# Kernel optimization log

Hardware: AMD Instinct MI355X
Metric: run time of the kernel (lower is better)

Reference implementation:

```python
import jax, jax.numpy as jnp
import numpy as np

DIM = 512
NL = 4
P = 8
B = 4
L = 8192  # byte-level sequence length
LP = L // P  # patch-level sequence length


def _ln(x, g, b, eps=1e-5):
    m = jnp.mean(x, axis=-1, keepdims=True)
    v = jnp.mean((x - m) ** 2, axis=-1, keepdims=True)
    return (x - m) * jax.lax.rsqrt(v + eps) * g + b


def setup_inputs() -> dict:
    key = jax.random.key(0)
    ks = jax.random.split(key, 24)
    s = 0.02
    inp = {
        "bytes_in": jax.random.randint(ks[0], (B, L), 0, 256, dtype=jnp.int32),
        "byte_emb": jax.random.normal(ks[1], (256, DIM), jnp.float32) * s,
        # patch encoder Conv1d(kernel=stride=P): weight laid out [P, D_in, D_out]
        "enc_w": jax.random.normal(ks[2], (P, DIM, DIM), jnp.float32) * s,
        "enc_b": jnp.zeros((DIM,), jnp.float32),
        "hash_proj": jax.random.normal(ks[3], (DIM, DIM), jnp.float32) * s,
        # per-layer stacked params
        "qkv_w": jax.random.normal(ks[4], (NL, DIM, 3 * DIM), jnp.float32) * s,
        "qkv_b": jnp.zeros((NL, 3 * DIM), jnp.float32),
        "gate_w": jax.random.normal(ks[5], (NL, DIM, DIM), jnp.float32) * s,
        "gate_b": jnp.zeros((NL, DIM), jnp.float32),
        "ln1_g": jnp.ones((NL, DIM), jnp.float32),
        "ln1_b": jnp.zeros((NL, DIM), jnp.float32),
        "mlp_w1": jax.random.normal(ks[6], (NL, DIM, 4 * DIM), jnp.float32) * s,
        "mlp_b1": jnp.zeros((NL, 4 * DIM), jnp.float32),
        "mlp_w2": jax.random.normal(ks[7], (NL, 4 * DIM, DIM), jnp.float32) * s,
        "mlp_b2": jnp.zeros((NL, DIM), jnp.float32),
        "ln2_g": jnp.ones((NL, DIM), jnp.float32),
        "ln2_b": jnp.zeros((NL, DIM), jnp.float32),
        # patch decoder ConvTranspose1d(kernel=stride=P): weight [D_in, P, D_out]
        "dec_w": jax.random.normal(ks[8], (DIM, P, DIM), jnp.float32) * s,
        "dec_b": jnp.zeros((DIM,), jnp.float32),
        "head_w": jax.random.normal(ks[9], (DIM, 256), jnp.float32) * s,
        "head_b": jnp.zeros((256,), jnp.float32),
    }
    return inp


def reference(bytes_in, byte_emb, enc_w, enc_b, hash_proj,
              qkv_w, qkv_b, gate_w, gate_b, ln1_g, ln1_b,
              mlp_w1, mlp_b1, mlp_w2, mlp_b2, ln2_g, ln2_b,
              dec_w, dec_b, head_w, head_b):
    # byte embedding: [B, L, D]
    x = byte_emb[bytes_in]
    # non-overlapping Conv1d(kernel=stride=P) == patch-wise contraction
    xp = x.reshape(B, LP, P, DIM)
    x = jnp.einsum('blpd,pdo->blo', xp, enc_w) + enc_b  # [B, LP, D]
    # hash projection
    x = x + jnp.tanh(x @ hash_proj)
    for i in range(NL):
        # LinearLatentKernel
        h = _ln(x, ln1_g[i], ln1_b[i])
        qkv = h @ qkv_w[i] + qkv_b[i]
        q, k, v = jnp.split(qkv, 3, axis=-1)
        kv_state = jnp.cumsum(k * v, axis=1)
        g = jax.nn.sigmoid(h @ gate_w[i] + gate_b[i])
        x = x + q * kv_state * g
        # MLP
        h = _ln(x, ln2_g[i], ln2_b[i])
        h = jax.nn.gelu(h @ mlp_w1[i] + mlp_b1[i], approximate=False)
        x = x + h @ mlp_w2[i] + mlp_b2[i]
    # ConvTranspose1d(kernel=stride=P): each patch expands to P positions
    y = jnp.einsum('bld,dpo->blpo', x, dec_w).reshape(B, L, DIM) + dec_b
    logits = y @ head_w + head_b  # [B, L, 256]
    return logits
```

## Files before the change

### kernel.cpp

```cpp
#include <hip/hip_runtime.h>
#include <hip/hip_bf16.h>
#include <math.h>

#define DIMD 512
#define NLAYER 4
#define PP 8
#define BBATCH 4
#define LBYTES 8192
#define LPATCH 1024
#define MROWS (BBATCH * LPATCH)

typedef __bf16 bf16x8 __attribute__((ext_vector_type(8)));
typedef float f32x4 __attribute__((ext_vector_type(4)));
typedef unsigned short u16x4 __attribute__((ext_vector_type(4)));
typedef unsigned short u16x8 __attribute__((ext_vector_type(8)));

__device__ __forceinline__ unsigned short f2bf(float f) {
    union { float f; unsigned u; } v; v.f = f;
    unsigned r = v.u + 0x7FFFu + ((v.u >> 16) & 1u);
    return (unsigned short)(r >> 16);
}
__device__ __forceinline__ float bf2f(unsigned short u) {
    union { unsigned u; float f; } v; v.u = ((unsigned)u) << 16;
    return v.f;
}

__device__ __forceinline__ void glds16(const unsigned short* g, unsigned short* l) {
    __builtin_amdgcn_global_load_lds((__attribute__((address_space(1))) void*)g,
                                     (__attribute__((address_space(3))) void*)l,
                                     16, 0, 0);
}

template<int TM, int ACT, bool BIAS, bool RES, bool OBF>
__global__ __launch_bounds__(256)
void mfma_gemm(const unsigned short* __restrict__ A, int lda, long aZ,
               const unsigned short* __restrict__ Bt, int ldb, long bZ,
               const float* __restrict__ bias,
               const float* __restrict__ res, int ldr,
               void* __restrict__ Cv, int ldc, long cZ, int K)
{
    constexpr int M_REP = TM / 32;
    __shared__ unsigned short As[TM * 32];
    __shared__ unsigned short Bs[128 * 32];

    const int tid = threadIdx.x;
    const int w = tid >> 6, l = tid & 63;
    const int row0 = blockIdx.x * TM;
    const int col0 = blockIdx.y * 128;
    A  += (size_t)blockIdx.z * aZ;
    Bt += (size_t)blockIdx.z * bZ;
    unsigned short* Cb = (unsigned short*)Cv + (size_t)blockIdx.z * cZ;
    float*          Cf = (float*)Cv          + (size_t)blockIdx.z * cZ;

    const int cA = w * 64 + l;
    const unsigned short* gA0 = A + (size_t)(row0 + (cA >> 2)) * lda + (cA & 3) * 8;
    const unsigned short* gB0 = Bt + (size_t)(col0 + (cA >> 2)) * ldb + (cA & 3) * 8;
    const unsigned short* gB1 = Bt + (size_t)(col0 + 64 + (cA >> 2)) * ldb + (cA & 3) * 8;
    unsigned short* lA0 = &As[w * 512];
    unsigned short* lB0 = &Bs[w * 512];
    unsigned short* lB1 = &Bs[2048 + w * 512];
    const unsigned short* gA1 = nullptr;
    unsigned short* lA1 = nullptr;
    if constexpr (TM == 128) {
        gA1 = A + (size_t)(row0 + 64 + (cA >> 2)) * lda + (cA & 3) * 8;
        lA1 = &As[2048 + w * 512];
    }

    const int wr = (w >> 1) * (TM / 2);
    const int wc = (w & 1) * 64;
    const int lr = l & 15, lk = (l >> 4) * 8;
    const int aBase = (wr + lr) * 32 + lk;
    const int bBase = (wc + lr) * 32 + lk;

    f32x4 acc[M_REP][4] = {};

    for (int k0 = 0; k0 < K; k0 += 32) {
        glds16(gA0, lA0);  gA0 += 32;
        if constexpr (TM == 128) { glds16(gA1, lA1); gA1 += 32; }
        glds16(gB0, lB0);  gB0 += 32;
        glds16(gB1, lB1);  gB1 += 32;
        __syncthreads();
        bf16x8 af[M_REP], bfr[4];
        #pragma unroll
        for (int m = 0; m < M_REP; m++)
            af[m] = *reinterpret_cast<const bf16x8*>(&As[aBase + m * 512]);
        #pragma unroll
        for (int n = 0; n < 4; n++)
            bfr[n] = *reinterpret_cast<const bf16x8*>(&Bs[bBase + n * 512]);
        #pragma unroll
        for (int m = 0; m < M_REP; m++)
            #pragma unroll
            for (int n = 0; n < 4; n++)
                acc[m][n] = __builtin_amdgcn_mfma_f32_16x16x32_bf16(
                    af[m], bfr[n], acc[m][n], 0, 0, 0);
        __syncthreads();
    }

    const int r0 = row0 + wr + (l >> 4) * 4;
    const int c0 = col0 + wc + lr;
    float bv[4] = {0.f, 0.f, 0.f, 0.f};
    if (BIAS) {
        #pragma unroll
        for (int n = 0; n < 4; n++) bv[n] = bias[c0 + n * 16];
    }
    #pragma unroll
    for (int m = 0; m < M_REP; m++) {
        #pragma unroll
        for (int j = 0; j < 4; j++) {
            const int row = r0 + m * 16 + j;
            #pragma unroll
            for (int n = 0; n < 4; n++) {
                float v = acc[m][n][j];
                if (BIAS) v += bv[n];
                if (ACT == 1) v = tanhf(v);
                if (ACT == 2) v = 0.5f * v * (1.f + erff(v * 0.70710678118f));
                if (RES) v += res[(size_t)row * ldr + c0 + n * 16];
                if (OBF) Cb[(size_t)row * ldc + c0 + n * 16] = f2bf(v);
                else     Cf[(size_t)row * ldc + c0 + n * 16] = v;
            }
        }
    }
}

__global__ __launch_bounds__(256)
void pack_t(const float* __restrict__ in, unsigned short* __restrict__ out,
            int K, int N, long inZ, long outZ)
{
    __shared__ float t[32][33];
    const int k0 = blockIdx.x * 32, n0 = blockIdx.y * 32;
    in  += (size_t)blockIdx.z * inZ;
    out += (size_t)blockIdx.z * outZ;
    const int tx = threadIdx.x & 31, ty = threadIdx.x >> 5;
    #pragma unroll
    for (int i = 0; i < 4; i++)
        t[ty + i * 8][tx] = in[(size_t)(k0 + ty + i * 8) * N + n0 + tx];
    __syncthreads();
    #pragma unroll
    for (int i = 0; i < 4; i++)
        out[(size_t)(n0 + ty + i * 8) * K + k0 + tx] = f2bf(t[tx][ty + i * 8]);
}

__global__ __launch_bounds__(256)
void ln_kernel(const float* __restrict__ x, const float* __restrict__ g,
               const float* __restrict__ b, unsigned short* __restrict__ h)
{
    const int row = blockIdx.x * 4 + (threadIdx.x >> 6);
    const int lane = threadIdx.x & 63;
    const float* xr = x + (long)row * DIMD;
    float4 v0 = *(const float4*)(xr + lane * 8);
    float4 v1 = *(const float4*)(xr + lane * 8 + 4);
    float xv[8] = {v0.x, v0.y, v0.z, v0.w, v1.x, v1.y, v1.z, v1.w};
    float s = 0.f, q = 0.f;
    #pragma unroll
    for (int j = 0; j < 8; j++) { s += xv[j]; q += xv[j] * xv[j]; }
    #pragma unroll
    for (int off = 1; off < 64; off <<= 1) {
        s += __shfl_xor(s, off);
        q += __shfl_xor(q, off);
    }
    const float mean = s * (1.f / DIMD);
    const float var  = q * (1.f / DIMD) - mean * mean;
    const float rstd = rsqrtf(var + 1e-5f);
    float4 g0 = *(const float4*)(g + lane * 8);
    float4 g1 = *(const float4*)(g + lane * 8 + 4);
    float4 b0 = *(const float4*)(b + lane * 8);
    float4 b1 = *(const float4*)(b + lane * 8 + 4);
    float gv[8] = {g0.x, g0.y, g0.z, g0.w, g1.x, g1.y, g1.z, g1.w};
    float bb[8] = {b0.x, b0.y, b0.z, b0.w, b1.x, b1.y, b1.z, b1.w};
    u16x8 o;
    #pragma unroll
    for (int j = 0; j < 8; j++) o[j] = f2bf((xv[j] - mean) * rstd * gv[j] + bb[j]);
    *reinterpret_cast<u16x8*>(h + (long)row * DIMD + lane * 8) = o;
}

__global__ __launch_bounds__(128)
void embed_kernel(const int* __restrict__ bytes, const float* __restrict__ E,
                  const float* __restrict__ enc_b, float* __restrict__ x0,
                  unsigned short* __restrict__ x0b)
{
    const int patch = blockIdx.x;
    __shared__ int by[PP];
    if (threadIdx.x < PP) by[threadIdx.x] = bytes[patch * PP + threadIdx.x];
    __syncthreads();
    const int o = threadIdx.x * 4;
    float4 acc = *(const float4*)(enc_b + o);
    #pragma unroll
    for (int p = 0; p < PP; p++) {
        float4 e = *(const float4*)(E + ((long)(p * 256 + by[p])) * DIMD + o);
        acc.x += e.x; acc.y += e.y; acc.z += e.z; acc.w += e.w;
    }
    *(float4*)(x0 + (long)patch * DIMD + o) = acc;
    u16x4 ob; ob[0] = f2bf(acc.x); ob[1] = f2bf(acc.y);
    ob[2] = f2bf(acc.z); ob[3] = f2bf(acc.w);
    *reinterpret_cast<u16x4*>(x0b + (long)patch * DIMD + o) = ob;
}

#define NCHUNK 64
#define CLEN   16
#define QGS    (4 * DIMD)

__global__ __launch_bounds__(512)
void scan_partial(const unsigned short* __restrict__ qg, float* __restrict__ S)
{
    const int b = blockIdx.x >> 6, c = blockIdx.x & 63, d = threadIdx.x;
    const unsigned short* base = qg + (long)(b * LPATCH + c * CLEN) * QGS;
    float s = 0.f;
    for (int l = 0; l < CLEN; l++) {
        float k = bf2f(base[l * QGS + DIMD + d]);
        float v = bf2f(base[l * QGS + 2 * DIMD + d]);
        s = fmaf(k, v, s);
    }
    S[(b * NCHUNK + c) * DIMD + d] = s;
}

__global__ __launch_bounds__(512)
void scan_prefix(float* __restrict__ S)
{
    const int b = blockIdx.x, d = threadIdx.x;
    float run = 0.f;
    for (int c = 0; c < NCHUNK; c++) {
        float v = S[(b * NCHUNK + c) * DIMD + d];
        S[(b * NCHUNK + c) * DIMD + d] = run;
        run += v;
    }
}

__global__ __launch_bounds__(512)
void scan_apply(const unsigned short* __restrict__ qg,
                const float* __restrict__ S, float* __restrict__ x)
{
    const int b = blockIdx.x >> 6, c = blockIdx.x & 63, d = threadIdx.x;
    float kv = S[(b * NCHUNK + c) * DIMD + d];
    const unsigned short* qb = qg + (long)(b * LPATCH + c * CLEN) * QGS;
    float* xb = x + (long)(b * LPATCH + c * CLEN) * DIMD;
    for (int l = 0; l < CLEN; l++) {
        float q = bf2f(qb[l * QGS + d]);
        float k = bf2f(qb[l * QGS + DIMD + d]);
        float v = bf2f(qb[l * QGS + 2 * DIMD + d]);
        float gp = bf2f(qb[l * QGS + 3 * DIMD + d]);
        kv = fmaf(k, v, kv);
        float g = 1.f / (1.f + expf(-gp));
        xb[l * DIMD + d] += q * kv * g;
    }
}

__global__ __launch_bounds__(256)
void catbias(const float* __restrict__ qb, const float* __restrict__ gb,
             float* __restrict__ cb)
{
    const int i = blockIdx.x >> 3;
    const int n = (blockIdx.x & 7) * 256 + threadIdx.x;
    cb[i * 2048 + n] = (n < 1536) ? qb[i * 1536 + n] : gb[i * 512 + n - 1536];
}

__global__ __launch_bounds__(256)
void fbias2(const unsigned short* __restrict__ hwT, const float* __restrict__ dec_b,
            const float* __restrict__ head_b, float* __restrict__ fb)
{
    const int w = threadIdx.x >> 6, l = threadIdx.x & 63;
    const int o = blockIdx.x * 4 + w;
    u16x8 hv = *reinterpret_cast<const u16x8*>(hwT + (size_t)o * DIMD + l * 8);
    float4 d0 = *(const float4*)(dec_b + l * 8);
    float4 d1 = *(const float4*)(dec_b + l * 8 + 4);
    float dd[8] = {d0.x, d0.y, d0.z, d0.w, d1.x, d1.y, d1.z, d1.w};
    float s = 0.f;
    #pragma unroll
    for (int j = 0; j < 8; j++) s += bf2f(hv[j]) * dd[j];
    #pragma unroll
    for (int off = 1; off < 64; off <<= 1) s += __shfl_xor(s, off);
    if (l == 0) {
        float v = s + head_b[o];
        #pragma unroll
        for (int p = 0; p < PP; p++) fb[p * 256 + o] = v;
    }
}

__global__ __launch_bounds__(256)
void cast_bf16(const float* __restrict__ in, unsigned short* __restrict__ out)
{
    const long i = (long)(blockIdx.x * 256 + threadIdx.x) * 8;
    float4 a = *(const float4*)(in + i);
    float4 b = *(const float4*)(in + i + 4);
    u16x8 o;
    o[0] = f2bf(a.x); o[1] = f2bf(a.y); o[2] = f2bf(a.z); o[3] = f2bf(a.w);
    o[4] = f2bf(b.x); o[5] = f2bf(b.y); o[6] = f2bf(b.z); o[7] = f2bf(b.w);
    *reinterpret_cast<u16x8*>(out + i) = o;
}

extern "C" void kernel_launch(void* const* d_in, const int* in_sizes, int n_in,
                              void* d_out, int out_size, void* d_ws, size_t ws_size,
                              hipStream_t stream)
{
    (void)in_sizes; (void)n_in; (void)out_size; (void)ws_size;

    const int*   bytes_in  = (const int*)d_in[0];
    const float* byte_emb  = (const float*)d_in[1];
    const float* enc_w     = (const float*)d_in[2];
    const float* enc_b     = (const float*)d_in[3];
    const float* hash_proj = (const float*)d_in[4];
    const float* qkv_w     = (const float*)d_in[5];
    const float* qkv_b     = (const float*)d_in[6];
    const float* gate_w    = (const float*)d_in[7];
    const float* gate_b    = (const float*)d_in[8];
    const float* ln1_g     = (const float*)d_in[9];
    const float* ln1_b     = (const float*)d_in[10];
    const float* mlp_w1    = (const float*)d_in[11];
    const float* mlp_b1    = (const float*)d_in[12];
    const float* mlp_w2    = (const float*)d_in[13];
    const float* mlp_b2    = (const float*)d_in[14];
    const float* ln2_g     = (const float*)d_in[15];
    const float* ln2_b     = (const float*)d_in[16];
    const float* dec_w     = (const float*)d_in[17];
    const float* dec_b     = (const float*)d_in[18];
    const float* head_w    = (const float*)d_in[19];
    const float* head_b    = (const float*)d_in[20];
    float* out = (float*)d_out;

    char* ws = (char*)d_ws;
    size_t o = 0;
    auto alloc = [&](size_t bytes) { char* p = ws + o; o += (bytes + 255) & ~(size_t)255; return p; };
    unsigned short* wcat   = (unsigned short*)alloc((size_t)4 * 2048 * 512 * 2);
    unsigned short* w1T    = (unsigned short*)alloc((size_t)4 * 2048 * 512 * 2);
    unsigned short* w2T    = (unsigned short*)alloc((size_t)4 * 512 * 2048 * 2);
    unsigned short* whashT = (unsigned short*)alloc((size_t)512 * 512 * 2);
    unsigned short* wWfT   = (unsigned short*)alloc((size_t)2048 * 512 * 2);
    unsigned short* encT   = (unsigned short*)alloc((size_t)8 * 512 * 512 * 2);
    unsigned short* hwT    = (unsigned short*)alloc((size_t)256 * 512 * 2);
    unsigned short* decb   = (unsigned short*)alloc((size_t)512 * 8 * 512 * 2);
    unsigned short* embB   = (unsigned short*)alloc((size_t)256 * 512 * 2);
    float* cbias           = (float*)alloc((size_t)4 * 2048 * 4);
    float* fb              = (float*)alloc(2048 * 4);
    float* E               = (float*)alloc((size_t)8 * 256 * 512 * 4);
    float* x               = (float*)alloc((size_t)MROWS * DIMD * 4);
    float* x0              = (float*)alloc((size_t)MROWS * DIMD * 4);
    unsigned short* x0b    = (unsigned short*)alloc((size_t)MROWS * DIMD * 2);
    unsigned short* h      = (unsigned short*)alloc((size_t)MROWS * DIMD * 2);
    unsigned short* xb     = (unsigned short*)alloc((size_t)MROWS * DIMD * 2);
    float* S               = (float*)alloc((size_t)BBATCH * NCHUNK * DIMD * 4);
    unsigned short* qg     = (unsigned short*)alloc((size_t)MROWS * 2048 * 2);
    unsigned short* hid    = (unsigned short*)alloc((size_t)MROWS * 2048 * 2);

    pack_t<<<dim3(16, 48, 4), 256, 0, stream>>>(qkv_w, wcat, 512, 1536,
        (long)512 * 1536, (long)2048 * 512);
    pack_t<<<dim3(16, 16, 4), 256, 0, stream>>>(gate_w, wcat + (size_t)1536 * 512, 512, 512,
        (long)512 * 512, (long)2048 * 512);
    pack_t<<<dim3(16, 64, 4), 256, 0, stream>>>(mlp_w1, w1T, 512, 2048,
        (long)512 * 2048, (long)2048 * 512);
    pack_t<<<dim3(64, 16, 4), 256, 0, stream>>>(mlp_w2, w2T, 2048, 512,
        (long)2048 * 512, (long)512 * 2048);
    pack_t<<<dim3(16, 16, 1), 256, 0, stream>>>(hash_proj, whashT, 512, 512, 0, 0);
    pack_t<<<dim3(16, 8, 1), 256, 0, stream>>>(head_w, hwT, 512, 256, 0, 0);
    pack_t<<<dim3(16, 16, 8), 256, 0, stream>>>(enc_w, encT, 512, 512,
        (long)512 * 512, (long)512 * 512);
    cast_bf16<<<dim3(1024), 256, 0, stream>>>(dec_w, decb);
    cast_bf16<<<dim3(64), 256, 0, stream>>>(byte_emb, embB);
    catbias<<<dim3(32), 256, 0, stream>>>(qkv_b, gate_b, cbias);

    mfma_gemm<64, 0, false, false, true><<<dim3(4, 4, 8), 256, 0, stream>>>(
        hwT, 512, 0L, decb, PP * 512, 512L,
        nullptr, nullptr, 0, wWfT, 512, (long)256 * 512, 512);
    fbias2<<<dim3(64), 256, 0, stream>>>(hwT, dec_b, head_b, fb);

    mfma_gemm<64, 0, false, false, false><<<dim3(4, 4, 8), 256, 0, stream>>>(
        embB, 512, 0L, encT, 512, (long)512 * 512,
        nullptr, nullptr, 0, E, 512, (long)256 * 512, 512);

    embed_kernel<<<dim3(MROWS), dim3(128), 0, stream>>>(bytes_in, E, enc_b, x0, x0b);

    mfma_gemm<64, 1, false, true, false><<<dim3(MROWS / 64, 4, 1), 256, 0, stream>>>(
        x0b, DIMD, 0L, whashT, DIMD, 0L, nullptr, x0, DIMD, x, DIMD, 0L, DIMD);

    for (int i = 0; i < NLAYER; i++) {
        ln_kernel<<<dim3(MROWS / 4), 256, 0, stream>>>(x, ln1_g + i * DIMD, ln1_b + i * DIMD, h);
        mfma_gemm<128, 0, true, false, true><<<dim3(MROWS / 128, 16, 1), 256, 0, stream>>>(
            h, DIMD, 0L, wcat + (size_t)i * 2048 * 512, DIMD, 0L,
            cbias + (size_t)i * 2048, nullptr, 0, qg, 2048, 0L, DIMD);
        scan_partial<<<dim3(BBATCH * NCHUNK), dim3(DIMD), 0, stream>>>(qg, S);
        scan_prefix<<<dim3(BBATCH), dim3(DIMD), 0, stream>>>(S);
        scan_apply<<<dim3(BBATCH * NCHUNK), dim3(DIMD), 0, stream>>>(qg, S, x);
        ln_kernel<<<dim3(MROWS / 4), 256, 0, stream>>>(x, ln2_g + i * DIMD, ln2_b + i * DIMD, h);
        mfma_gemm<128, 2, true, false, true><<<dim3(MROWS / 128, 16, 1), 256, 0, stream>>>(
            h, DIMD, 0L, w1T + (size_t)i * 2048 * 512, DIMD, 0L,
            mlp_b1 + (size_t)i * 2048, nullptr, 0, hid, 2048, 0L, DIMD);
        if (i < NLAYER - 1) {
            mfma_gemm<64, 0, true, true, false><<<dim3(MROWS / 64, 4, 1), 256, 0, stream>>>(
                hid, 2048, 0L, w2T + (size_t)i * 512 * 2048, 2048, 0L,
                mlp_b2 + (size_t)i * DIMD, x, DIMD, x, DIMD, 0L, 2048);
        } else {
            mfma_gemm<64, 0, true, true, true><<<dim3(MROWS / 64, 4, 1), 256, 0, stream>>>(
                hid, 2048, 0L, w2T + (size_t)i * 512 * 2048, 2048, 0L,
                mlp_b2 + (size_t)i * DIMD, x, DIMD, xb, DIMD, 0L, 2048);
        }
    }

    mfma_gemm<128, 0, true, false, false><<<dim3(MROWS / 128, 16, 1), 256, 0, stream>>>(
        xb, DIMD, 0L, wWfT, DIMD, 0L, fb, nullptr, 0, out, 2048, 0L, DIMD);
}
```

Baseline: 483.4 us.

## Merge weight-packing launches and fuse scan prefix, apply and LayerNorm

Ten setup kernels (transposes, casts, bias concat) become one megapack launch that dispatches on block index. Inside each layer, the separate chunk-prefix kernel is removed: each apply block sums the earlier chunk partials itself. The second LayerNorm is fused into the scan-apply kernel using a block reduction per row, and the scan kernels now handle two channels per thread with 256 threads. This cuts launch count and one full read/write pass over x per layer, in exchange for redundant prefix summation and two block syncs per row.

Result: slower. 531.3 us (+9.9%).

```diff
diff --git a/kernel.cpp b/kernel.cpp
--- a/kernel.cpp
+++ b/kernel.cpp
@@ -9,6 +9,10 @@
 #define LBYTES 8192
 #define LPATCH 1024
 #define MROWS (BBATCH * LPATCH)
+
+#define NCHUNK 64
+#define CLEN   16
+#define QGS    (4 * DIMD)
 
 typedef __bf16 bf16x8 __attribute__((ext_vector_type(8)));
 typedef float f32x4 __attribute__((ext_vector_type(4)));
@@ -122,14 +126,12 @@
     }
 }
 
-__global__ __launch_bounds__(256)
-void pack_t(const float* __restrict__ in, unsigned short* __restrict__ out,
-            int K, int N, long inZ, long outZ)
-{
-    __shared__ float t[32][33];
-    const int k0 = blockIdx.x * 32, n0 = blockIdx.y * 32;
-    in  += (size_t)blockIdx.z * inZ;
-    out += (size_t)blockIdx.z * outZ;
+__device__ __forceinline__ void packT_body(float* sm, const float* __restrict__ in,
+                                           unsigned short* __restrict__ out,
+                                           int K, int N, int bx, int by)
+{
+    float (*t)[33] = (float(*)[33])sm;
+    const int k0 = bx * 32, n0 = by * 32;
     const int tx = threadIdx.x & 31, ty = threadIdx.x >> 5;
     #pragma unroll
     for (int i = 0; i < 4; i++)
@@ -138,6 +140,72 @@
     #pragma unroll
     for (int i = 0; i < 4; i++)
         out[(size_t)(n0 + ty + i * 8) * K + k0 + tx] = f2bf(t[tx][ty + i * 8]);
+}
+
+__device__ __forceinline__ void cast_body(const float* __restrict__ in,
+                                          unsigned short* __restrict__ out, int blk)
+{
+    const long i = ((long)blk * 256 + threadIdx.x) * 8;
+    float4 a = *(const float4*)(in + i);
+    float4 b = *(const float4*)(in + i + 4);
+    u16x8 o;
+    o[0] = f2bf(a.x); o[1] = f2bf(a.y); o[2] = f2bf(a.z); o[3] = f2bf(a.w);
+    o[4] = f2bf(b.x); o[5] = f2bf(b.y); o[6] = f2bf(b.z); o[7] = f2bf(b.w);
+    *reinterpret_cast<u16x8*>(out + i) = o;
+}
+
+__global__ __launch_bounds__(256)
+void megapack(const float* __restrict__ qkv_w, const float* __restrict__ gate_w,
+              const float* __restrict__ mlp_w1, const float* __restrict__ mlp_w2,
+              const float* __restrict__ hash_proj, const float* __restrict__ head_w,
+              const float* __restrict__ enc_w, const float* __restrict__ dec_w,
+              const float* __restrict__ byte_emb,
+              const float* __restrict__ qkv_b, const float* __restrict__ gate_b,
+              unsigned short* __restrict__ wcat, unsigned short* __restrict__ w1T,
+              unsigned short* __restrict__ w2T, unsigned short* __restrict__ whashT,
+              unsigned short* __restrict__ hwT, unsigned short* __restrict__ encT,
+              unsigned short* __restrict__ decb, unsigned short* __restrict__ embB,
+              float* __restrict__ cbias)
+{
+    __shared__ float sm[32 * 33];
+    int id = blockIdx.x;
+    if (id < 3072) {
+        int z = id / 768, r = id % 768;
+        packT_body(sm, qkv_w + (size_t)z * 512 * 1536, wcat + (size_t)z * 2048 * 512,
+                   512, 1536, r % 16, r / 16);
+    } else if (id < 4096) {
+        id -= 3072; int z = id / 256, r = id % 256;
+        packT_body(sm, gate_w + (size_t)z * 512 * 512,
+                   wcat + (size_t)z * 2048 * 512 + (size_t)1536 * 512,
+                   512, 512, r % 16, r / 16);
+    } else if (id < 8192) {
+        id -= 4096; int z = id / 1024, r = id % 1024;
+        packT_body(sm, mlp_w1 + (size_t)z * 512 * 2048, w1T + (size_t)z * 2048 * 512,
+                   512, 2048, r % 16, r / 16);
+    } else if (id < 12288) {
+        id -= 8192; int z = id / 1024, r = id % 1024;
+        packT_body(sm, mlp_w2 + (size_t)z * 2048 * 512, w2T + (size_t)z * 512 * 2048,
+                   2048, 512, r % 64, r / 64);
+    } else if (id < 12544) {
+        id -= 12288;
+        packT_body(sm, hash_proj, whashT, 512, 512, id % 16, id / 16);
+    } else if (id < 12672) {
+        id -= 12544;
+        packT_body(sm, head_w, hwT, 512, 256, id % 16, id / 16);
+    } else if (id < 14720) {
+        id -= 12672; int z = id / 256, r = id % 256;
+        packT_body(sm, enc_w + (size_t)z * 512 * 512, encT + (size_t)z * 512 * 512,
+                   512, 512, r % 16, r / 16);
+    } else if (id < 15744) {
+        cast_body(dec_w, decb, id - 14720);
+    } else if (id < 15808) {
+        cast_body(byte_emb, embB, id - 15744);
+    } else {
+        id -= 15808;
+        const int i = id >> 3;
+        const int n = (id & 7) * 256 + threadIdx.x;
+        cbias[i * 2048 + n] = (n < 1536) ? qkv_b[i * 1536 + n] : gate_b[i * 512 + n - 1536];
+    }
 }
 
 __global__ __launch_bounds__(256)
@@ -195,62 +263,76 @@
     *reinterpret_cast<u16x4*>(x0b + (long)patch * DIMD + o) = ob;
 }
 
-#define NCHUNK 64
-#define CLEN   16
-#define QGS    (4 * DIMD)
-
-__global__ __launch_bounds__(512)
+__global__ __launch_bounds__(256)
 void scan_partial(const unsigned short* __restrict__ qg, float* __restrict__ S)
 {
-    const int b = blockIdx.x >> 6, c = blockIdx.x & 63, d = threadIdx.x;
-    const unsigned short* base = qg + (long)(b * LPATCH + c * CLEN) * QGS;
-    float s = 0.f;
+    const int b = blockIdx.x >> 6, c = blockIdx.x & 63, d2 = threadIdx.x * 2;
+    const unsigned short* base = qg + (size_t)(b * LPATCH + c * CLEN) * QGS;
+    float s0 = 0.f, s1 = 0.f;
     for (int l = 0; l < CLEN; l++) {
-        float k = bf2f(base[l * QGS + DIMD + d]);
-        float v = bf2f(base[l * QGS + 2 * DIMD + d]);
-        s = fmaf(k, v, s);
-    }
-    S[(b * NCHUNK + c) * DIMD + d] = s;
-}
-
-__global__ __launch_bounds__(512)
-void scan_prefix(float* __restrict__ S)
-{
-    const int b = blockIdx.x, d = threadIdx.x;
-    float run = 0.f;
-    for (int c = 0; c < NCHUNK; c++) {
-        float v = S[(b * NCHUNK + c) * DIMD + d];
-        S[(b * NCHUNK + c) * DIMD + d] = run;
-        run += v;
-    }
-}
-
-__global__ __launch_bounds__(512)
-void scan_apply(const unsigned short* __restrict__ qg,
-                const float* __restrict__ S, float* __restrict__ x)
-{
-    const int b = blockIdx.x >> 6, c = blockIdx.x & 63, d = threadIdx.x;
-    float kv = S[(b * NCHUNK + c) * DIMD + d];
-    const unsigned short* qb = qg + (long)(b * LPATCH + c * CLEN) * QGS;
-    float* xb = x + (long)(b * LPATCH + c * CLEN) * DIMD;
+        ushort2 kk = *(const ushort2*)(base + l * QGS + DIMD + d2);
+        ushort2 vv = *(const ushort2*)(base + l * QGS + 2 * DIMD + d2);
+        s0 = fmaf(bf2f(kk.x), bf2f(vv.x), s0);
+        s1 = fmaf(bf2f(kk.y), bf2f(vv.y), s1);
+    }
+    *(float2*)(S + (size_t)(b * NCHUNK + c) * DIMD + d2) = make_float2(s0, s1);
+}
+
+__global__ __launch_bounds__(256)
+void scan_apply_ln(const unsigned short* __restrict__ qg,
+                   const float* __restrict__ S, float* __restrict__ x,
+                   const float* __restrict__ lg, const float* __restrict__ lb,
+                   unsigned short* __restrict__ h)
+{
+    const int b = blockIdx.x >> 6, c = blockIdx.x & 63;
+    const int t = threadIdx.x, d2 = t * 2;
+    const int wid = t >> 6, lane = t & 63;
+
+    float kv0 = 0.f, kv1 = 0.f;
+    const float* Sb = S + (size_t)b * NCHUNK * DIMD;
+    for (int j = 0; j < c; j++) {
+        float2 sv = *(const float2*)(Sb + j * DIMD + d2);
+        kv0 += sv.x; kv1 += sv.y;
+    }
+    const float g0 = lg[d2], g1 = lg[d2 + 1];
+    const float b0 = lb[d2], b1 = lb[d2 + 1];
+    const int row0 = b * LPATCH + c * CLEN;
+    __shared__ float redS[4], redQ[4];
+
     for (int l = 0; l < CLEN; l++) {
-        float q = bf2f(qb[l * QGS + d]);
-        float k = bf2f(qb[l * QGS + DIMD + d]);
-        float v = bf2f(qb[l * QGS + 2 * DIMD + d]);
-        float gp = bf2f(qb[l * QGS + 3 * DIMD + d]);
-        kv = fmaf(k, v, kv);
-        float g = 1.f / (1.f + expf(-gp));
-        xb[l * DIMD + d] += q * kv * g;
-    }
-}
-
-__global__ __launch_bounds__(256)
-void catbias(const float* __restrict__ qb, const float* __restrict__ gb,
-             float* __restrict__ cb)
-{
-    const int i = blockIdx.x >> 3;
-    const int n = (blockIdx.x & 7) * 256 + threadIdx.x;
-    cb[i * 2048 + n] = (n < 1536) ? qb[i * 1536 + n] : gb[i * 512 + n - 1536];
+        const unsigned short* qb = qg + (size_t)(row0 + l) * QGS;
+        ushort2 qq = *(const ushort2*)(qb + d2);
+        ushort2 kk = *(const ushort2*)(qb + DIMD + d2);
+        ushort2 vv = *(const ushort2*)(qb + 2 * DIMD + d2);
+        ushort2 gg = *(const ushort2*)(qb + 3 * DIMD + d2);
+        kv0 = fmaf(bf2f(kk.x), bf2f(vv.x), kv0);
+        kv1 = fmaf(bf2f(kk.y), bf2f(vv.y), kv1);
+        const float sg0 = 1.f / (1.f + expf(-bf2f(gg.x)));
+        const float sg1 = 1.f / (1.f + expf(-bf2f(gg.y)));
+        float* xr = x + (size_t)(row0 + l) * DIMD;
+        float2 xv = *(const float2*)(xr + d2);
+        const float n0 = xv.x + bf2f(qq.x) * kv0 * sg0;
+        const float n1 = xv.y + bf2f(qq.y) * kv1 * sg1;
+        *(float2*)(xr + d2) = make_float2(n0, n1);
+
+        float s = n0 + n1, qs = n0 * n0 + n1 * n1;
+        #pragma unroll
+        for (int off = 1; off < 64; off <<= 1) {
+            s += __shfl_xor(s, off); qs += __shfl_xor(qs, off);
+        }
+        if (lane == 0) { redS[wid] = s; redQ[wid] = qs; }
+        __syncthreads();
+        const float ts = redS[0] + redS[1] + redS[2] + redS[3];
+        const float tq = redQ[0] + redQ[1] + redQ[2] + redQ[3];
+        __syncthreads();
+        const float mean = ts * (1.f / DIMD);
+        const float var  = tq * (1.f / DIMD) - mean * mean;
+        const float rstd = rsqrtf(var + 1e-5f);
+        ushort2 ho;
+        ho.x = f2bf((n0 - mean) * rstd * g0 + b0);
+        ho.y = f2bf((n1 - mean) * rstd * g1 + b1);
+        *(ushort2*)(h + (size_t)(row0 + l) * DIMD + d2) = ho;
+    }
 }
 
 __global__ __launch_bounds__(256)
@@ -273,18 +355,6 @@
         #pragma unroll
         for (int p = 0; p < PP; p++) fb[p * 256 + o] = v;
     }
-}
-
-__global__ __launch_bounds__(256)
-void cast_bf16(const float* __restrict__ in, unsigned short* __restrict__ out)
-{
-    const long i = (long)(blockIdx.x * 256 + threadIdx.x) * 8;
-    float4 a = *(const float4*)(in + i);
-    float4 b = *(const float4*)(in + i + 4);
-    u16x8 o;
-    o[0] = f2bf(a.x); o[1] = f2bf(a.y); o[2] = f2bf(a.z); o[3] = f2bf(a.w);
-    o[4] = f2bf(b.x); o[5] = f2bf(b.y); o[6] = f2bf(b.z); o[7] = f2bf(b.w);
-    *reinterpret_cast<u16x8*>(out + i) = o;
 }
 
 extern "C" void kernel_launch(void* const* d_in, const int* in_sizes, int n_in,
@@ -340,21 +410,10 @@
     unsigned short* qg     = (unsigned short*)alloc((size_t)MROWS * 2048 * 2);
     unsigned short* hid    = (unsigned short*)alloc((size_t)MROWS * 2048 * 2);
 
-    pack_t<<<dim3(16, 48, 4), 256, 0, stream>>>(qkv_w, wcat, 512, 1536,
-        (long)512 * 1536, (long)2048 * 512);
-    pack_t<<<dim3(16, 16, 4), 256, 0, stream>>>(gate_w, wcat + (size_t)1536 * 512, 512, 512,
-        (long)512 * 512, (long)2048 * 512);
-    pack_t<<<dim3(16, 64, 4), 256, 0, stream>>>(mlp_w1, w1T, 512, 2048,
-        (long)512 * 2048, (long)2048 * 512);
-    pack_t<<<dim3(64, 16, 4), 256, 0, stream>>>(mlp_w2, w2T, 2048, 512,
-        (long)2048 * 512, (long)512 * 2048);
-    pack_t<<<dim3(16, 16, 1), 256, 0, stream>>>(hash_proj, whashT, 512, 512, 0, 0);
-    pack_t<<<dim3(16, 8, 1), 256, 0, stream>>>(head_w, hwT, 512, 256, 0, 0);
-    pack_t<<<dim3(16, 16, 8), 256, 0, stream>>>(enc_w, encT, 512, 512,
-        (long)512 * 512, (long)512 * 512);
-    cast_bf16<<<dim3(1024), 256, 0, stream>>>(dec_w, decb);
-    cast_bf16<<<dim3(64), 256, 0, stream>>>(byte_emb, embB);
-    catbias<<<dim3(32), 256, 0, stream>>>(qkv_b, gate_b, cbias);
+    megapack<<<dim3(15840), 256, 0, stream>>>(
+        qkv_w, gate_w, mlp_w1, mlp_w2, hash_proj, head_w, enc_w, dec_w, byte_emb,
+        qkv_b, gate_b,
+        wcat, w1T, w2T, whashT, hwT, encT, decb, embB, cbias);
 
     mfma_gemm<64, 0, false, false, true><<<dim3(4, 4, 8), 256, 0, stream>>>(
         hwT, 512, 0L, decb, PP * 512, 512L,
@@ -375,10 +434,9 @@
         mfma_gemm<128, 0, true, false, true><<<dim3(MROWS / 128, 16, 1), 256, 0, stream>>>(
             h, DIMD, 0L, wcat + (size_t)i * 2048 * 512, DIMD, 0L,
             cbias + (size_t)i * 2048, nullptr, 0, qg, 2048, 0L, DIMD);
-        scan_partial<<<dim3(BBATCH * NCHUNK), dim3(DIMD), 0, stream>>>(qg, S);
-        scan_prefix<<<dim3(BBATCH), dim3(DIMD), 0, stream>>>(S);
-        scan_apply<<<dim3(BBATCH * NCHUNK), dim3(DIMD), 0, stream>>>(qg, S, x);
-        ln_kernel<<<dim3(MROWS / 4), 256, 0, stream>>>(x, ln2_g + i * DIMD, ln2_b + i * DIMD, h);
+        scan_partial<<<dim3(BBATCH * NCHUNK), 256, 0, stream>>>(qg, S);
+        scan_apply_ln<<<dim3(BBATCH * NCHUNK), 256, 0, stream>>>(
+            qg, S, x, ln2_g + i * DIMD, ln2_b + i * DIMD, h);
         mfma_gemm<128, 2, true, false, true><<<dim3(MROWS / 128, 16, 1), 256, 0, stream>>>(
             h, DIMD, 0L, w1T + (size_t)i * 2048 * 512, DIMD, 0L,
             mlp_b1 + (size_t)i * 2048, nullptr, 0, hid, 2048, 0L, DIMD);
```
